# Optimization experiments

Hardware: AMD Instinct MI355X
Metric: run time of the kernel (lower is better)

## Reference

```python
import jax, jax.numpy as jnp
import numpy as np

N_EMBD = 1024
N_HEAD = 16
HEAD_DIM = N_EMBD // N_HEAD


def setup_inputs() -> dict:
    key = jax.random.key(0)
    kx, kq, kk, kv, kp = jax.random.split(key, 5)
    B, S = 4, 2048
    x = jax.random.normal(kx, (B, S, N_EMBD), dtype=jnp.float32)
    # nn.Linear(n, n, bias=False): weight [out, in], y = x @ W.T
    s = 1.0 / np.sqrt(N_EMBD)
    Wq = jax.random.uniform(kq, (N_EMBD, N_EMBD), jnp.float32, -s, s)
    Wk = jax.random.uniform(kk, (N_EMBD, N_EMBD), jnp.float32, -s, s)
    Wv = jax.random.uniform(kv, (N_EMBD, N_EMBD), jnp.float32, -s, s)
    Wo = jax.random.uniform(kp, (N_EMBD, N_EMBD), jnp.float32, -s, s)
    return {"x": x, "Wq": Wq, "Wk": Wk, "Wv": Wv, "Wo": Wo}


def _split_heads(t):
    B, S, _ = t.shape
    return t.reshape(B, S, N_HEAD, HEAD_DIM).transpose(0, 2, 1, 3)  # [B,H,S,D]


def reference(x, Wq, Wk, Wv, Wo):
    q = _split_heads(x @ Wq.T)
    k = _split_heads(x @ Wk.T)
    v = _split_heads(x @ Wv.T)
    scale = 1.0 / np.sqrt(HEAD_DIM)
    scores = jnp.einsum('bhqd,bhkd->bhqk', q, k) * scale  # [B,H,S,S]
    S = x.shape[1]
    mask = jnp.tril(jnp.ones((S, S), dtype=bool))
    masked = jnp.where(mask[None, None], scores, -jnp.inf)
    attn = jax.nn.softmax(masked, axis=-1)
    heads = jnp.einsum('bhqk,bhkd->bhqd', attn, v)
    merged = heads.transpose(0, 2, 1, 3).reshape(x.shape[0], S, N_EMBD)
    return merged @ Wo.T
```

## Files before the change

kernel.cpp:

```cpp
#include <hip/hip_runtime.h>
#include <hip/hip_bf16.h>

typedef __hip_bfloat16 bf16;
typedef __attribute__((ext_vector_type(8))) short short8;
typedef __attribute__((ext_vector_type(4))) float f32x4;
typedef unsigned int uint32;

#define MFMA16(a, b, c) __builtin_amdgcn_mfma_f32_16x16x32_bf16(a, b, c, 0, 0, 0)

constexpr int EMB   = 1024;
constexpr int SEQ   = 2048;
constexpr int BATCH = 4;
constexpr int NH    = 16;
constexpr int HD    = 64;
constexpr int QKVW  = 3 * EMB;
constexpr float QSCALE = 0.125f * 1.44269504f;

__device__ __forceinline__ void gl_lds16(const bf16* g, bf16* l) {
    __builtin_amdgcn_global_load_lds(
        (const __attribute__((address_space(1))) void*)g,
        (__attribute__((address_space(3))) void*)l,
        16, 0, 0);
}

__device__ __forceinline__ float fexp2(float x) {
#if __has_builtin(__builtin_amdgcn_exp2f)
    return __builtin_amdgcn_exp2f(x);
#else
    return exp2f(x);
#endif
}

__device__ __forceinline__ uint32 pack2(float a, float b) {
    uint32 ua = __builtin_bit_cast(uint32, a) + 0x8000u;
    uint32 ub = __builtin_bit_cast(uint32, b) + 0x8000u;
    return __builtin_amdgcn_perm(ub, ua, 0x07060302u);
}

__device__ __forceinline__ bf16 fbf16(float f) {
    unsigned short u =
        (unsigned short)((__builtin_bit_cast(uint32, f) + 0x8000u) >> 16);
    return __builtin_bit_cast(bf16, u);
}

__device__ __forceinline__ int ps_dw(int row, int cd) {
    return row * 64 + ((((cd >> 2) ^ (row & 7)) << 3) + ((cd & 3) << 1));
}

__global__ void convert_all(const float* __restrict__ x,
                            const float* __restrict__ wq,
                            const float* __restrict__ wk,
                            const float* __restrict__ wv,
                            const float* __restrict__ wo,
                            bf16* __restrict__ xc,
                            bf16* __restrict__ wqkv,
                            bf16* __restrict__ woc) {
    const int NX = BATCH * SEQ * EMB;
    const int NW = EMB * EMB;
    const float* src; bf16* dst; int n4, b0, nb;
    const int blk = blockIdx.x;
    if (blk < 2048)      { src = x;  dst = xc;          n4 = NX / 4; b0 = 0;    nb = 2048; }
    else if (blk < 2304) { src = wq; dst = wqkv;        n4 = NW / 4; b0 = 2048; nb = 256; }
    else if (blk < 2560) { src = wk; dst = wqkv + NW;   n4 = NW / 4; b0 = 2304; nb = 256; }
    else if (blk < 2816) { src = wv; dst = wqkv + 2*NW; n4 = NW / 4; b0 = 2560; nb = 256; }
    else                 { src = wo; dst = woc;         n4 = NW / 4; b0 = 2816; nb = 256; }
    for (int i = (blk - b0) * 256 + threadIdx.x; i < n4; i += nb * 256) {
        float4 v = ((const float4*)src)[i];
        uint2 o;
        o.x = pack2(v.x, v.y);
        o.y = pack2(v.z, v.w);
        ((uint2*)dst)[i] = o;
    }
}

template <typename OutT>
__global__ __launch_bounds__(256) void gemm_bt(const bf16* __restrict__ A,
                                               const bf16* __restrict__ B,
                                               OutT* __restrict__ C,
                                               int M, int N, int K,
                                               float oscale, int qlim) {
    __shared__ __align__(16) bf16 As[128 * 64];
    __shared__ __align__(16) bf16 Bs[128 * 64];

    const int t    = threadIdx.x;
    const int lane = t & 63;
    const int wid  = t >> 6;
    const int l16  = lane & 15;
    const int quad = lane >> 4;
    const int e    = l16 & 7;
    const int wm   = (wid >> 1) * 64;
    const int wn   = (wid & 1) * 64;

    const int nwg = (int)gridDim.x;
    const int cpx = nwg >> 3;
    const int wg  = ((int)blockIdx.x & 7) * cpx + ((int)blockIdx.x >> 3);
    const int gx  = N >> 7;
    const int m0  = (wg / gx) * 128;
    const int n0  = (wg % gx) * 128;
    const float sc = (n0 < qlim) ? oscale : 1.0f;

    f32x4 acc[4][4] = {};
    const int srow = lane >> 3;
    const int scol = ((lane & 7) ^ srow) * 8;

    for (int k0 = 0; k0 < K; k0 += 64) {
        #pragma unroll
        for (int it = 0; it < 4; ++it) {
            int rb = it * 32 + wid * 8;
            gl_lds16(&A[(size_t)(m0 + rb + srow) * K + k0 + scol], &As[rb * 64]);
            gl_lds16(&B[(size_t)(n0 + rb + srow) * K + k0 + scol], &Bs[rb * 64]);
        }
        __syncthreads();
        #pragma unroll
        for (int ks = 0; ks < 64; ks += 32) {
            const int cb = (ks >> 3) + quad;
            short8 af[4], bfr[4];
            #pragma unroll
            for (int i = 0; i < 4; ++i)
                af[i] = *(const short8*)&As[(wm + i * 16 + l16) * 64 + ((cb ^ e) * 8)];
            #pragma unroll
            for (int j = 0; j < 4; ++j)
                bfr[j] = *(const short8*)&Bs[(wn + j * 16 + l16) * 64 + ((cb ^ e) * 8)];
            #pragma unroll
            for (int i = 0; i < 4; ++i)
                #pragma unroll
                for (int j = 0; j < 4; ++j)
                    acc[i][j] = MFMA16(af[i], bfr[j], acc[i][j]);
        }
        __syncthreads();
    }

    #pragma unroll
    for (int i = 0; i < 4; ++i)
        #pragma unroll
        for (int j = 0; j < 4; ++j)
            #pragma unroll
            for (int r = 0; r < 4; ++r) {
                int row = m0 + wm + i * 16 + quad * 4 + r;
                int col = n0 + wn + j * 16 + l16;
                float v = acc[i][j][r] * sc;
                if constexpr (sizeof(OutT) == 2)
                    C[(size_t)row * N + col] = fbf16(v);
                else
                    C[(size_t)row * N + col] = (OutT)v;
            }
}

__global__ __launch_bounds__(256) void transpose_v(const bf16* __restrict__ QKV,
                                                   bf16* __restrict__ Vt) {
    __shared__ __align__(16) bf16 Ts[4096];
    const int t  = threadIdx.x;
    const int st = blockIdx.x;
    const int bh = blockIdx.y;
    const int b  = bh >> 4, h = bh & 15;
    const int s0 = st * 64;

    const bf16* src = QKV + ((size_t)(b * SEQ + s0)) * QKVW + 2 * EMB + h * HD;
    {
        int r = t >> 3, cq = t & 7;
        #pragma unroll
        for (int it = 0; it < 2; ++it, r += 32) {
            uint4 v = *(const uint4*)&src[(size_t)r * QKVW + cq * 8];
            int blk = cq ^ (r >> 3);
            *(uint4*)&Ts[r * 64 + blk * 8] = v;
        }
    }
    __syncthreads();
    bf16* dst = Vt + (size_t)bh * HD * SEQ + s0;
    {
        int d = t >> 3;
        const int sq = t & 7;
        #pragma unroll
        for (int it = 0; it < 2; ++it, d += 32) {
            short8 ov;
            #pragma unroll
            for (int i = 0; i < 8; ++i) {
                int s = sq * 8 + i;
                ov[i] = (short)__bfloat16_as_ushort(
                    Ts[s * 64 + (((d >> 3) ^ sq) << 3) + (d & 7)]);
            }
            *(short8*)&dst[(size_t)d * SEQ + sq * 8] = ov;
        }
    }
}

__global__ __launch_bounds__(256) void flash_attn(const bf16* __restrict__ QKV,
                                                  const bf16* __restrict__ Vt,
                                                  bf16* __restrict__ O) {
    __shared__ __align__(16) bf16 Ks[2][64 * 64];
    __shared__ __align__(16) bf16 VTs[2][64 * 64];
    __shared__ __align__(16) bf16 Ps[4][16 * 64];

    const int t    = threadIdx.x;
    const int lane = t & 63;
    const int w    = t >> 6;
    const int l16  = lane & 15;
    const int quad = lane >> 4;
    const int e    = l16 & 7;

    const int lin = (int)blockIdx.x;
    const int wg  = ((lin & 7) << 7) + (lin >> 3);
    const int bh  = wg >> 4;
    const int qt  = wg & 15;
    const int b   = bh >> 4, h = bh & 15;
    const int q0  = qt * 128;

    const bf16* Qp = QKV + (size_t)b * SEQ * QKVW + h * HD;
    const bf16* Kp = QKV + (size_t)b * SEQ * QKVW + EMB + h * HD;
    const bf16* Vp = Vt + (size_t)bh * HD * SEQ;

    short8 bQ[2][2];
    #pragma unroll
    for (int s = 0; s < 2; ++s) {
        const size_t qr = (size_t)(q0 + w * 32 + s * 16 + l16) * QKVW;
        bQ[s][0] = *(const short8*)&Qp[qr + quad * 8];
        bQ[s][1] = *(const short8*)&Qp[qr + 32 + quad * 8];
    }

    f32x4 o[2][4] = {};
    float lrow[2] = {0.f, 0.f};

    const int ntiles = q0 / 64 + 2;
    const int srow = lane >> 3;
    const int scol = ((lane & 7) ^ srow) * 8;

    auto stage = [&](int kt, int buf) {
        const int kbase = kt * 64;
        #pragma unroll
        for (int it = 0; it < 2; ++it) {
            int rb = it * 32 + w * 8;
            gl_lds16(&Kp[(size_t)(kbase + rb + srow) * QKVW + scol], &Ks[buf][rb * 64]);
            gl_lds16(&Vp[(size_t)(rb + srow) * SEQ + kbase + scol], &VTs[buf][rb * 64]);
        }
    };

    stage(0, 0);
    stage(1, 1);

    for (int kt = 0; kt < ntiles; ++kt) {
        const int cur = kt & 1;
        const int kbase = kt * 64;
        if (kt < ntiles - 1) __builtin_amdgcn_s_waitcnt(0x0F74);
        else                 __builtin_amdgcn_s_waitcnt(0x0F70);
        __builtin_amdgcn_s_barrier();

        #pragma unroll
        for (int s = 0; s < 2; ++s) {
            const int qs0 = q0 + w * 32 + s * 16;
            if (kbase > qs0 + 15) continue;

            f32x4 sa[4];
            #pragma unroll
            for (int j = 0; j < 4; ++j) {
                f32x4 acc = {};
                acc = MFMA16(*(const short8*)&Ks[cur][(j * 16 + l16) * 64 + ((quad ^ e) * 8)],
                             bQ[s][0], acc);
                acc = MFMA16(*(const short8*)&Ks[cur][(j * 16 + l16) * 64 + (((4 + quad) ^ e) * 8)],
                             bQ[s][1], acc);
                sa[j] = acc;
            }

            float lsum = 0.f;
            if (kbase + 63 > qs0) {
                #pragma unroll
                for (int j = 0; j < 4; ++j)
                    #pragma unroll
                    for (int pr = 0; pr < 2; ++pr) {
                        int kg = kbase + j * 16 + quad * 4 + 2 * pr;
                        float e0 = fexp2(sa[j][2 * pr]);
                        float e1 = fexp2(sa[j][2 * pr + 1]);
                        float p0 = (kg     <= qs0 + l16) ? e0 : 0.f;
                        float p1 = (kg + 1 <= qs0 + l16) ? e1 : 0.f;
                        lsum += p0 + p1;
                        *(uint32*)&Ps[w][ps_dw(l16, j * 8 + quad * 2 + pr)] = pack2(p0, p1);
                    }
            } else {
                #pragma unroll
                for (int j = 0; j < 4; ++j)
                    #pragma unroll
                    for (int pr = 0; pr < 2; ++pr) {
                        float p0 = fexp2(sa[j][2 * pr]);
                        float p1 = fexp2(sa[j][2 * pr + 1]);
                        lsum += p0 + p1;
                        *(uint32*)&Ps[w][ps_dw(l16, j * 8 + quad * 2 + pr)] = pack2(p0, p1);
                    }
            }
            lrow[s] += lsum;

            #pragma unroll
            for (int ks = 0; ks < 2; ++ks) {
                short8 bP = *(const short8*)&Ps[w][l16 * 64 + (((ks * 4 + quad) ^ e) << 3)];
                #pragma unroll
                for (int dg = 0; dg < 4; ++dg)
                    o[s][dg] = MFMA16(
                        *(const short8*)&VTs[cur][(dg * 16 + l16) * 64 + (((ks * 4 + quad) ^ e) * 8)],
                        bP, o[s][dg]);
            }
        }

        __builtin_amdgcn_s_barrier();
        if (kt + 2 < ntiles) stage(kt + 2, cur);
    }

    bf16* Op = O + (size_t)b * SEQ * EMB + h * HD;
    #pragma unroll
    for (int s = 0; s < 2; ++s) {
        float l = lrow[s];
        l += __shfl_xor(l, 16);
        l += __shfl_xor(l, 32);
        float rl = 1.0f / l;
        #pragma unroll
        for (int dg = 0; dg < 4; ++dg)
            #pragma unroll
            for (int pr = 0; pr < 2; ++pr) {
                float v0 = o[s][dg][2 * pr] * rl;
                float v1 = o[s][dg][2 * pr + 1] * rl;
                *(uint32*)&Ps[w][ps_dw(l16, dg * 8 + quad * 2 + pr)] = pack2(v0, v1);
            }
        #pragma unroll
        for (int it = 0; it < 2; ++it) {
            int qr = lane >> 2;
            int ch = (lane & 3) + 4 * it;
            short8 vv = *(const short8*)&Ps[w][qr * 64 + ((ch ^ (qr & 7)) << 3)];
            *(short8*)&Op[(size_t)(q0 + w * 32 + s * 16 + qr) * EMB + ch * 8] = vv;
        }
    }
}

extern "C" void kernel_launch(void* const* d_in, const int* in_sizes, int n_in,
                              void* d_out, int out_size, void* d_ws, size_t ws_size,
                              hipStream_t stream) {
    const float* x  = (const float*)d_in[0];
    const float* Wq = (const float*)d_in[1];
    const float* Wk = (const float*)d_in[2];
    const float* Wv = (const float*)d_in[3];
    const float* Wo = (const float*)d_in[4];
    float* out = (float*)d_out;
    bf16*  ws  = (bf16*)d_ws;

    const int M  = BATCH * SEQ;
    const int NX = M * EMB;
    const int NW = EMB * EMB;

    bf16* xc   = ws;
    bf16* Ab   = xc;
    bf16* Wqkv = ws + (size_t)NX;
    bf16* Woc  = Wqkv + 3 * (size_t)NW;
    bf16* QKV  = Woc + NW;
    bf16* Vt   = QKV + (size_t)M * QKVW;

    convert_all<<<3072, 256, 0, stream>>>(x, Wq, Wk, Wv, Wo, xc, Wqkv, Woc);

    gemm_bt<bf16><<<dim3((QKVW / 128) * (M / 128)), 256, 0, stream>>>(
        xc, Wqkv, QKV, M, QKVW, EMB, QSCALE, EMB);

    transpose_v<<<dim3(SEQ / 64, BATCH * NH), 256, 0, stream>>>(QKV, Vt);

    flash_attn<<<dim3((SEQ / 128) * BATCH * NH), 256, 0, stream>>>(QKV, Vt, Ab);

    gemm_bt<float><<<dim3((EMB / 128) * (M / 128)), 256, 0, stream>>>(
        Ab, Woc, out, M, EMB, EMB, 1.0f, 0);
}
```

Before: 256.3 us.

## Pair causal query tiles per block to balance flash attention work

Each attention block now processes two query tiles, a long one (15-pr) and a short one (pr), in sequence, and the grid is halved. This equalizes the triangular causal workload across blocks to reduce tail imbalance. The cost is fewer blocks in flight and a serialized second pass with its own pipeline prologue, which may lower latency hiding.

```diff
diff --git a/kernel.cpp b/kernel.cpp
--- a/kernel.cpp
+++ b/kernel.cpp
@@ -199,28 +199,16 @@
     const int e    = l16 & 7;
 
     const int lin = (int)blockIdx.x;
-    const int wg  = ((lin & 7) << 7) + (lin >> 3);
-    const int bh  = wg >> 4;
-    const int qt  = wg & 15;
+    const int wg  = ((lin & 7) << 6) + (lin >> 3);
+    const int bh  = wg >> 3;
+    const int pr  = wg & 7;
     const int b   = bh >> 4, h = bh & 15;
-    const int q0  = qt * 128;
 
     const bf16* Qp = QKV + (size_t)b * SEQ * QKVW + h * HD;
     const bf16* Kp = QKV + (size_t)b * SEQ * QKVW + EMB + h * HD;
     const bf16* Vp = Vt + (size_t)bh * HD * SEQ;
-
-    short8 bQ[2][2];
-    #pragma unroll
-    for (int s = 0; s < 2; ++s) {
-        const size_t qr = (size_t)(q0 + w * 32 + s * 16 + l16) * QKVW;
-        bQ[s][0] = *(const short8*)&Qp[qr + quad * 8];
-        bQ[s][1] = *(const short8*)&Qp[qr + 32 + quad * 8];
-    }
-
-    f32x4 o[2][4] = {};
-    float lrow[2] = {0.f, 0.f};
-
-    const int ntiles = q0 / 64 + 2;
+    bf16* Op = O + (size_t)b * SEQ * EMB + h * HD;
+
     const int srow = lane >> 3;
     const int scol = ((lane & 7) ^ srow) * 8;
 
@@ -234,95 +222,112 @@
         }
     };
 
-    stage(0, 0);
-    stage(1, 1);
-
-    for (int kt = 0; kt < ntiles; ++kt) {
-        const int cur = kt & 1;
-        const int kbase = kt * 64;
-        if (kt < ntiles - 1) __builtin_amdgcn_s_waitcnt(0x0F74);
-        else                 __builtin_amdgcn_s_waitcnt(0x0F70);
-        __builtin_amdgcn_s_barrier();
-
+    for (int pass = 0; pass < 2; ++pass) {
+        const int qt = pass ? pr : 15 - pr;
+        const int q0 = qt * 128;
+
+        short8 bQ[2][2];
         #pragma unroll
         for (int s = 0; s < 2; ++s) {
-            const int qs0 = q0 + w * 32 + s * 16;
-            if (kbase > qs0 + 15) continue;
-
-            f32x4 sa[4];
-            #pragma unroll
-            for (int j = 0; j < 4; ++j) {
-                f32x4 acc = {};
-                acc = MFMA16(*(const short8*)&Ks[cur][(j * 16 + l16) * 64 + ((quad ^ e) * 8)],
-                             bQ[s][0], acc);
-                acc = MFMA16(*(const short8*)&Ks[cur][(j * 16 + l16) * 64 + (((4 + quad) ^ e) * 8)],
-                             bQ[s][1], acc);
-                sa[j] = acc;
+            const size_t qr = (size_t)(q0 + w * 32 + s * 16 + l16) * QKVW;
+            bQ[s][0] = *(const short8*)&Qp[qr + quad * 8];
+            bQ[s][1] = *(const short8*)&Qp[qr + 32 + quad * 8];
+        }
+
+        f32x4 o[2][4] = {};
+        float lrow[2] = {0.f, 0.f};
+
+        const int ntiles = q0 / 64 + 2;
+
+        stage(0, 0);
+        stage(1, 1);
+
+        for (int kt = 0; kt < ntiles; ++kt) {
+            const int cur = kt & 1;
+            const int kbase = kt * 64;
+            if (kt < ntiles - 1) __builtin_amdgcn_s_waitcnt(0x0F74);
+            else                 __builtin_amdgcn_s_waitcnt(0x0F70);
+            __builtin_amdgcn_s_barrier();
+
+            #pragma unroll
+            for (int s = 0; s < 2; ++s) {
+                const int qs0 = q0 + w * 32 + s * 16;
+                if (kbase > qs0 + 15) continue;
+
+                f32x4 sa[4];
+                #pragma unroll
+                for (int j = 0; j < 4; ++j) {
+                    f32x4 acc = {};
+                    acc = MFMA16(*(const short8*)&Ks[cur][(j * 16 + l16) * 64 + ((quad ^ e) * 8)],
+                                 bQ[s][0], acc);
+                    acc = MFMA16(*(const short8*)&Ks[cur][(j * 16 + l16) * 64 + (((4 + quad) ^ e) * 8)],
+                                 bQ[s][1], acc);
+                    sa[j] = acc;
+                }
+
+                float lsum = 0.f;
+                if (kbase + 63 > qs0) {
+                    #pragma unroll
+                    for (int j = 0; j < 4; ++j)
+                        #pragma unroll
+                        for (int pp = 0; pp < 2; ++pp) {
+                            int kg = kbase + j * 16 + quad * 4 + 2 * pp;
+                            float e0 = fexp2(sa[j][2 * pp]);
+                            float e1 = fexp2(sa[j][2 * pp + 1]);
+                            float p0 = (kg     <= qs0 + l16) ? e0 : 0.f;
+                            float p1 = (kg + 1 <= qs0 + l16) ? e1 : 0.f;
+                            lsum += p0 + p1;
+                            *(uint32*)&Ps[w][ps_dw(l16, j * 8 + quad * 2 + pp)] = pack2(p0, p1);
+                        }
+                } else {
+                    #pragma unroll
+                    for (int j = 0; j < 4; ++j)
+                        #pragma unroll
+                        for (int pp = 0; pp < 2; ++pp) {
+                            float p0 = fexp2(sa[j][2 * pp]);
+                            float p1 = fexp2(sa[j][2 * pp + 1]);
+                            lsum += p0 + p1;
+                            *(uint32*)&Ps[w][ps_dw(l16, j * 8 + quad * 2 + pp)] = pack2(p0, p1);
+                        }
+                }
+                lrow[s] += lsum;
+
+                #pragma unroll
+                for (int ks = 0; ks < 2; ++ks) {
+                    short8 bP = *(const short8*)&Ps[w][l16 * 64 + (((ks * 4 + quad) ^ e) << 3)];
+                    #pragma unroll
+                    for (int dg = 0; dg < 4; ++dg)
+                        o[s][dg] = MFMA16(
+                            *(const short8*)&VTs[cur][(dg * 16 + l16) * 64 + (((ks * 4 + quad) ^ e) * 8)],
+                            bP, o[s][dg]);
+                }
             }
 
-            float lsum = 0.f;
-            if (kbase + 63 > qs0) {
+            __builtin_amdgcn_s_barrier();
+            if (kt + 2 < ntiles) stage(kt + 2, cur);
+        }
+
+        #pragma unroll
+        for (int s = 0; s < 2; ++s) {
+            float l = lrow[s];
+            l += __shfl_xor(l, 16);
+            l += __shfl_xor(l, 32);
+            float rl = 1.0f / l;
+            #pragma unroll
+            for (int dg = 0; dg < 4; ++dg)
                 #pragma unroll
-                for (int j = 0; j < 4; ++j)
-                    #pragma unroll
-                    for (int pr = 0; pr < 2; ++pr) {
-                        int kg = kbase + j * 16 + quad * 4 + 2 * pr;
-                        float e0 = fexp2(sa[j][2 * pr]);
-                        float e1 = fexp2(sa[j][2 * pr + 1]);
-                        float p0 = (kg     <= qs0 + l16) ? e0 : 0.f;
-                        float p1 = (kg + 1 <= qs0 + l16) ? e1 : 0.f;
-                        lsum += p0 + p1;
-                        *(uint32*)&Ps[w][ps_dw(l16, j * 8 + quad * 2 + pr)] = pack2(p0, p1);
-                    }
-            } else {
-                #pragma unroll
-                for (int j = 0; j < 4; ++j)
-                    #pragma unroll
-                    for (int pr = 0; pr < 2; ++pr) {
-                        float p0 = fexp2(sa[j][2 * pr]);
-                        float p1 = fexp2(sa[j][2 * pr + 1]);
-                        lsum += p0 + p1;
-                        *(uint32*)&Ps[w][ps_dw(l16, j * 8 + quad * 2 + pr)] = pack2(p0, p1);
-                    }
+                for (int pp = 0; pp < 2; ++pp) {
+                    float v0 = o[s][dg][2 * pp] * rl;
+                    float v1 = o[s][dg][2 * pp + 1] * rl;
+                    *(uint32*)&Ps[w][ps_dw(l16, dg * 8 + quad * 2 + pp)] = pack2(v0, v1);
+                }
+            #pragma unroll
+            for (int it = 0; it < 2; ++it) {
+                int qr = lane >> 2;
+                int ch = (lane & 3) + 4 * it;
+                short8 vv = *(const short8*)&Ps[w][qr * 64 + ((ch ^ (qr & 7)) << 3)];
+                *(short8*)&Op[(size_t)(q0 + w * 32 + s * 16 + qr) * EMB + ch * 8] = vv;
             }
-            lrow[s] += lsum;
-
-            #pragma unroll
-            for (int ks = 0; ks < 2; ++ks) {
-                short8 bP = *(const short8*)&Ps[w][l16 * 64 + (((ks * 4 + quad) ^ e) << 3)];
-                #pragma unroll
-                for (int dg = 0; dg < 4; ++dg)
-                    o[s][dg] = MFMA16(
-                        *(const short8*)&VTs[cur][(dg * 16 + l16) * 64 + (((ks * 4 + quad) ^ e) * 8)],
-                        bP, o[s][dg]);
-            }
-        }
-
-        __builtin_amdgcn_s_barrier();
-        if (kt + 2 < ntiles) stage(kt + 2, cur);
-    }
-
-    bf16* Op = O + (size_t)b * SEQ * EMB + h * HD;
-    #pragma unroll
-    for (int s = 0; s < 2; ++s) {
-        float l = lrow[s];
-        l += __shfl_xor(l, 16);
-        l += __shfl_xor(l, 32);
-        float rl = 1.0f / l;
-        #pragma unroll
-        for (int dg = 0; dg < 4; ++dg)
-            #pragma unroll
-            for (int pr = 0; pr < 2; ++pr) {
-                float v0 = o[s][dg][2 * pr] * rl;
-                float v1 = o[s][dg][2 * pr + 1] * rl;
-                *(uint32*)&Ps[w][ps_dw(l16, dg * 8 + quad * 2 + pr)] = pack2(v0, v1);
-            }
-        #pragma unroll
-        for (int it = 0; it < 2; ++it) {
-            int qr = lane >> 2;
-            int ch = (lane & 3) + 4 * it;
-            short8 vv = *(const short8*)&Ps[w][qr * 64 + ((ch ^ (qr & 7)) << 3)];
-            *(short8*)&Op[(size_t)(q0 + w * 32 + s * 16 + qr) * EMB + ch * 8] = vv;
         }
     }
 }
@@ -356,7 +361,7 @@
 
     transpose_v<<<dim3(SEQ / 64, BATCH * NH), 256, 0, stream>>>(QKV, Vt);
 
-    flash_attn<<<dim3((SEQ / 128) * BATCH * NH), 256, 0, stream>>>(QKV, Vt, Ab);
+    flash_attn<<<dim3((SEQ / 128) * BATCH * NH / 2), 256, 0, stream>>>(QKV, Vt, Ab);
 
     gemm_bt<float><<<dim3((EMB / 128) * (M / 128)), 256, 0, stream>>>(
         Ab, Woc, out, M, EMB, EMB, 1.0f, 0);
```

Measured after the change: 247.6 us. 1.04x faster.
